# Kernel tuning notes

Measured on AMD Instinct MI355X. Metric: run time of the kernel, lower is better.

Reference implementation:

```python
import jax, jax.numpy as jnp
import numpy as np

EMB_DIM = 1024
NUM_HEAD = 16
HEAD_DIM = EMB_DIM // NUM_HEAD
B, S = 2, 2048


def setup_inputs() -> dict:
    key = jax.random.key(0)
    ks = jax.random.split(key, 10)
    scale = 1.0 / np.sqrt(EMB_DIM)
    x = jax.random.normal(ks[0], (B, S, EMB_DIM), dtype=jnp.float32)
    # causal mask: 1 = keep, 0 = masked out (torch masked_fill(mask == 0, -inf))
    mask = jnp.tril(jnp.ones((S, S), dtype=jnp.int32))[None, None, :, :]
    def lin(kw, kb):
        W = jax.random.uniform(kw, (EMB_DIM, EMB_DIM), jnp.float32, -scale, scale)
        b = jax.random.uniform(kb, (EMB_DIM,), jnp.float32, -scale, scale)
        return W, b
    Wq, bq = lin(ks[1], ks[2])
    Wk, bk = lin(ks[3], ks[4])
    Wv, bv = lin(ks[5], ks[6])
    Wo, bo = lin(ks[7], ks[8])
    return {"x": x, "mask": mask, "Wq": Wq, "bq": bq, "Wk": Wk, "bk": bk,
            "Wv": Wv, "bv": bv, "Wo": Wo, "bo": bo}


def reference(x, mask, Wq, bq, Wk, bk, Wv, bv, Wo, bo):
    Bsz, Sq, _ = x.shape
    # projections; torch Linear: y = x @ W^T + b
    def proj(W, b):
        y = jnp.einsum('bse,fe->bsf', x, W) + b
        return y.reshape(Bsz, Sq, NUM_HEAD, HEAD_DIM).transpose(0, 2, 1, 3)  # [B,H,S,D]
    q = proj(Wq, bq)
    k = proj(Wk, bk)
    v = proj(Wv, bv)
    scaling = jnp.asarray(HEAD_DIM ** 0.5, x.dtype)
    scores = jnp.einsum('bhqd,bhkd->bhqk', q, k) / scaling  # [B,H,S,S]
    scores = jnp.where(mask == 0, -jnp.inf, scores)
    attn = jax.nn.softmax(scores, axis=-1)
    out = jnp.einsum('bhqk,bhkd->bhqd', attn, v)
    out = out.transpose(0, 2, 1, 3).reshape(Bsz, Sq, EMB_DIM)
    return jnp.einsum('bse,fe->bsf', out, Wo) + bo
```

## Files before the change

kernel.cpp:

```cpp
#include <hip/hip_runtime.h>

typedef unsigned short u16;
typedef __attribute__((ext_vector_type(8))) __bf16 bf16x8;
typedef __attribute__((ext_vector_type(8))) short  short8;
typedef __attribute__((ext_vector_type(4))) short  short4v;
typedef __attribute__((ext_vector_type(4))) float  floatx4;
typedef __attribute__((ext_vector_type(4))) int    intx4;
typedef __attribute__((ext_vector_type(2))) int    intx2;

constexpr int Bc = 2, Sc = 2048, Ec = 1024, Hc = 16, Dc = 64;
constexpr int Mc = Bc * Sc;

#define QSCALE  0.18033688011112042f

__device__ __forceinline__ u16 f2b(float f) {
  union { float f; unsigned u; } c; c.f = f;
  unsigned u = c.u;
  return (u16)((u + 0x7fffu + ((u >> 16) & 1u)) >> 16);
}
__device__ __forceinline__ short8 ld8(const u16* p) { return *(const short8*)p; }

__device__ __forceinline__ int cvt_pk(float lo, float hi) {
  int r;
  asm("v_cvt_pk_bf16_f32 %0, %1, %2" : "=v"(r) : "v"(lo), "v"(hi));
  return r;
}

__device__ __forceinline__ floatx4 mfma16(short8 a, short8 b, floatx4 c) {
  return __builtin_amdgcn_mfma_f32_16x16x32_bf16(
      __builtin_bit_cast(bf16x8, a), __builtin_bit_cast(bf16x8, b), c, 0, 0, 0);
}

__device__ __forceinline__ void async16(const u16* g, u16* l) {
  __builtin_amdgcn_global_load_lds(
      (const __attribute__((address_space(1))) void*)g,
      (__attribute__((address_space(3))) void*)l, 16, 0, 0);
}

__global__ __launch_bounds__(256) void cvt_kernel(
    const float* __restrict__ x,  const float* __restrict__ Wq,
    const float* __restrict__ Wk, const float* __restrict__ Wv,
    const float* __restrict__ Wo, u16* __restrict__ dst) {
  const size_t i = ((size_t)blockIdx.x * 256 + threadIdx.x) * 4;
  const int seg = (int)(i >> 20);
  const float* src;
  size_t off;
  if (seg < 4)       { src = x;  off = i; }
  else if (seg == 4) { src = Wq; off = i - ((size_t)4 << 20); }
  else if (seg == 5) { src = Wk; off = i - ((size_t)5 << 20); }
  else if (seg == 6) { src = Wv; off = i - ((size_t)6 << 20); }
  else               { src = Wo; off = i - ((size_t)7 << 20); }
  floatx4 v = *(const floatx4*)(src + off);
  intx2 o;
  o[0] = cvt_pk(v[0], v[1]);
  o[1] = cvt_pk(v[2], v[3]);
  *(intx2*)(dst + i) = o;
}

__device__ __forceinline__ void gemm128d(
    const u16* __restrict__ A, const u16* __restrict__ B, int K,
    int m0, int n0, u16* As, u16* Bs, floatx4 acc[4][4]) {
  const int t = threadIdx.x;
  const int w = t >> 6, lane = t & 63;
  const int wm = w & 1, wn = w >> 1;
  const int quad = lane >> 4, l16 = lane & 15;
  const int r = t >> 2;
  const int c = ((t & 3) ^ ((t >> 3) & 3)) * 8;
  const int rs = (quad ^ ((l16 >> 1) & 3)) * 8;

  const u16* ap0 = A + (size_t)(m0 + r) * K + c;
  const u16* ap1 = A + (size_t)(m0 + 64 + r) * K + c;
  const u16* bp0 = B + (size_t)(n0 + r) * K + c;
  const u16* bp1 = B + (size_t)(n0 + 64 + r) * K + c;
  u16* const al0 = As + w * 512;
  u16* const al1 = As + 2048 + w * 512;
  u16* const bl0 = Bs + w * 512;
  u16* const bl1 = Bs + 2048 + w * 512;

#pragma unroll
  for (int i = 0; i < 4; ++i)
#pragma unroll
    for (int j = 0; j < 4; ++j) acc[i][j] = 0.f;

  async16(ap0, al0);
  async16(ap1, al1);
  async16(bp0, bl0);
  async16(bp1, bl1);

  int cur = 0;
  for (int k0 = 0; k0 < K; k0 += 32) {
    if (k0 + 32 < K) {
      const int nb = cur ^ 1;
      async16(ap0 + k0 + 32, al0 + nb * 4096);
      async16(ap1 + k0 + 32, al1 + nb * 4096);
      async16(bp0 + k0 + 32, bl0 + nb * 4096);
      async16(bp1 + k0 + 32, bl1 + nb * 4096);
      __builtin_amdgcn_sched_barrier(0);
      asm volatile("s_waitcnt vmcnt(4)");
    } else {
      asm volatile("s_waitcnt vmcnt(0)");
    }
    __builtin_amdgcn_s_barrier();
    __builtin_amdgcn_sched_barrier(0);

    short8 af[4], bfr[4];
#pragma unroll
    for (int i = 0; i < 4; ++i)
      af[i]  = *(const short8*)(As + cur * 4096 +
                                (wm * 64 + i * 16 + l16) * 32 + rs);
#pragma unroll
    for (int j = 0; j < 4; ++j)
      bfr[j] = *(const short8*)(Bs + cur * 4096 +
                                (wn * 64 + j * 16 + l16) * 32 + rs);
#pragma unroll
    for (int i = 0; i < 4; ++i)
#pragma unroll
      for (int j = 0; j < 4; ++j)
        acc[i][j] = mfma16(af[i], bfr[j], acc[i][j]);

    __builtin_amdgcn_sched_barrier(0);
    __builtin_amdgcn_s_barrier();
    cur ^= 1;
  }
}

__device__ __forceinline__ void gemm64x128(
    const u16* __restrict__ A, const u16* __restrict__ B, int K,
    int m0, int n0, u16* As, u16* Bs, floatx4 acc[2][4]) {
  const int t = threadIdx.x;
  const int w = t >> 6, lane = t & 63;
  const int wm = w & 1, wn = w >> 1;
  const int quad = lane >> 4, l16 = lane & 15;
  const int r = t >> 2;
  const int c = ((t & 3) ^ ((t >> 3) & 3)) * 8;
  const int rs = (quad ^ ((l16 >> 1) & 3)) * 8;

  const u16* ap  = A + (size_t)(m0 + r) * K + c;
  const u16* bp0 = B + (size_t)(n0 + r) * K + c;
  const u16* bp1 = B + (size_t)(n0 + 64 + r) * K + c;
  u16* const al  = As + w * 512;
  u16* const bl0 = Bs + w * 512;
  u16* const bl1 = Bs + 2048 + w * 512;

#pragma unroll
  for (int i = 0; i < 2; ++i)
#pragma unroll
    for (int j = 0; j < 4; ++j) acc[i][j] = 0.f;

  async16(ap,  al);
  async16(bp0, bl0);
  async16(bp1, bl1);

  int cur = 0;
  for (int k0 = 0; k0 < K; k0 += 32) {
    if (k0 + 32 < K) {
      const int nb = cur ^ 1;
      async16(ap  + k0 + 32, al  + nb * 2048);
      async16(bp0 + k0 + 32, bl0 + nb * 4096);
      async16(bp1 + k0 + 32, bl1 + nb * 4096);
      __builtin_amdgcn_sched_barrier(0);
      asm volatile("s_waitcnt vmcnt(3)");
    } else {
      asm volatile("s_waitcnt vmcnt(0)");
    }
    __builtin_amdgcn_s_barrier();
    __builtin_amdgcn_sched_barrier(0);

    short8 af[2], bfr[4];
#pragma unroll
    for (int i = 0; i < 2; ++i)
      af[i]  = *(const short8*)(As + cur * 2048 +
                                (wm * 32 + i * 16 + l16) * 32 + rs);
#pragma unroll
    for (int j = 0; j < 4; ++j)
      bfr[j] = *(const short8*)(Bs + cur * 4096 +
                                (wn * 64 + j * 16 + l16) * 32 + rs);
#pragma unroll
    for (int i = 0; i < 2; ++i)
#pragma unroll
      for (int j = 0; j < 4; ++j)
        acc[i][j] = mfma16(af[i], bfr[j], acc[i][j]);

    __builtin_amdgcn_sched_barrier(0);
    __builtin_amdgcn_s_barrier();
    cur ^= 1;
  }
}

__global__ __launch_bounds__(256, 4) void qkv_mm(
    const u16* __restrict__ xb, const u16* __restrict__ Wb,
    const float* __restrict__ bq, const float* __restrict__ bk,
    const float* __restrict__ bv,
    u16* __restrict__ Q, u16* __restrict__ K_, u16* __restrict__ Vt) {
  __shared__ __align__(16) u16 As[8192], Bs[8192];
  const int z = blockIdx.z;
  const u16* W = Wb + ((size_t)z << 20);
  const float* bias = (z == 0) ? bq : (z == 1) ? bk : bv;
  const int m0 = blockIdx.y * 128, n0 = blockIdx.x * 128;

  floatx4 acc[4][4];
  gemm128d(xb, W, Ec, m0, n0, As, Bs, acc);

  const int t = threadIdx.x, w = t >> 6, lane = t & 63;
  const int wm = w & 1, wn = w >> 1, quad = lane >> 4, l16 = lane & 15;
#pragma unroll
  for (int i = 0; i < 4; ++i)
#pragma unroll
    for (int j = 0; j < 4; ++j)
#pragma unroll
      for (int rr = 0; rr < 4; ++rr) {
        const int row = m0 + wm * 64 + i * 16 + quad * 4 + rr;
        const int col = n0 + wn * 64 + j * 16 + l16;
        float v = acc[i][j][rr] + bias[col];
        if (z == 0) v *= QSCALE;
        const int bb = row >> 11, s = row & (Sc - 1);
        const int h = col >> 6, d = col & (Dc - 1), bh = bb * Hc + h;
        if (z < 2) ((z == 0) ? Q : K_)[((size_t)bh * Sc + s) * Dc + d] = f2b(v);
        else {
          const int sp = (s & ~31) | ((s & 12) << 1) | ((s & 16) >> 2) | (s & 3);
          Vt[((size_t)bh * Dc + d) * Sc + sp] = f2b(v);
        }
      }
}

__global__ __launch_bounds__(256, 6) void proj_mm(
    const u16* __restrict__ O, const u16* __restrict__ Wob,
    const float* __restrict__ bias, float* __restrict__ out) {
  __shared__ __align__(16) u16 As[4096], Bs[8192];
  const int m0 = blockIdx.y * 64, n0 = blockIdx.x * 128;

  floatx4 acc[2][4];
  gemm64x128(O, Wob, Ec, m0, n0, As, Bs, acc);

  const int t = threadIdx.x, w = t >> 6, lane = t & 63;
  const int wm = w & 1, wn = w >> 1, quad = lane >> 4, l16 = lane & 15;
#pragma unroll
  for (int i = 0; i < 2; ++i)
#pragma unroll
    for (int j = 0; j < 4; ++j)
#pragma unroll
      for (int rr = 0; rr < 4; ++rr) {
        const int row = m0 + wm * 32 + i * 16 + quad * 4 + rr;
        const int col = n0 + wn * 64 + j * 16 + l16;
        out[(size_t)row * Ec + col] = acc[i][j][rr] + bias[col];
      }
}

__global__ __launch_bounds__(512, 4) void attn_kernel(
    const u16* __restrict__ Q, const u16* __restrict__ K,
    const u16* __restrict__ Vt, u16* __restrict__ O) {
  const int id = blockIdx.x;
  int qt, bh;
  if (id < 256) { qt = id & 15;        bh = id >> 4; }
  else          { qt = 15 - (id & 15); bh = 16 + ((id - 256) >> 4); }
  const int q0 = qt * 128;
  const int bb = bh >> 4, h = bh & 15;

  const u16* Qh = Q  + (size_t)bh * Sc * Dc;
  const u16* Kh = K  + (size_t)bh * Sc * Dc;
  const u16* Vh = Vt + (size_t)bh * Dc * Sc;

  const int t = threadIdx.x;
  const int w = t >> 6, lane = t & 63;
  const int quad = lane >> 4, l16 = lane & 15;

  __shared__ __align__(16) u16 Ks[8192];
  __shared__ __align__(16) u16 Vs[8192];

  const int sr = w * 8 + (lane >> 3);
  const int sb = (lane & 7) ^ (lane >> 3);
  const int swz = l16 & 7;

  const u16* qrow_p = Qh + (size_t)(q0 + w * 16 + l16) * Dc;
  const short8 aq0 = ld8(qrow_p + quad * 8);
  const short8 aq1 = ld8(qrow_p + 32 + quad * 8);

  float   lrow = 0.f;
  floatx4 oacc[4];
#pragma unroll
  for (int dt = 0; dt < 4; ++dt) oacc[dt] = 0.f;

  for (int kt = 0; kt <= q0; kt += 128) {
#pragma unroll
    for (int st = 0; st < 2; ++st) {
      async16(Kh + (size_t)(kt + st * 64 + sr) * Dc + sb * 8,
              Ks + st * 4096 + w * 512);
      async16(Vh + (size_t)sr * Sc + kt + st * 64 + sb * 8,
              Vs + st * 4096 + w * 512);
    }
    __syncthreads();

    floatx4 sacc[8];
#pragma unroll
    for (int g = 0; g < 8; ++g) sacc[g] = 0.f;
    __builtin_amdgcn_s_setprio(1);
#pragma unroll
    for (int ks = 0; ks < 2; ++ks) {
      const short8 bq = ks ? aq1 : aq0;
#pragma unroll
      for (int g = 0; g < 8; ++g) {
        const short8 a = *(const short8*)(
            Ks + (g >> 2) * 4096 + ((g & 3) * 16 + l16) * 64 +
            (((ks * 4 + quad) ^ swz) * 8));
        sacc[g] = mfma16(a, bq, sacc[g]);
      }
    }
    __builtin_amdgcn_s_setprio(0);

    const bool diag = (kt == q0);
    const int thr = q0 + w * 16 + l16 - kt - 4 * quad;
#pragma unroll
    for (int g = 0; g < 8; ++g)
#pragma unroll
      for (int r = 0; r < 4; ++r) {
        float pv = exp2f(sacc[g][r]);
        if (diag && (16 * g + r > thr)) pv = 0.f;
        lrow += pv;
        sacc[g][r] = pv;
      }

    short8 pa[4];
#pragma unroll
    for (int c = 0; c < 4; ++c) {
      intx4 wd;
      wd[0] = cvt_pk(sacc[2 * c][0],     sacc[2 * c][1]);
      wd[1] = cvt_pk(sacc[2 * c][2],     sacc[2 * c][3]);
      wd[2] = cvt_pk(sacc[2 * c + 1][0], sacc[2 * c + 1][1]);
      wd[3] = cvt_pk(sacc[2 * c + 1][2], sacc[2 * c + 1][3]);
      pa[c] = __builtin_bit_cast(short8, wd);
    }

    __builtin_amdgcn_s_setprio(1);
#pragma unroll
    for (int c = 0; c < 4; ++c) {
      const int st = c >> 1, kcl = c & 1;
#pragma unroll
      for (int dt = 0; dt < 4; ++dt) {
        const short8 b = *(const short8*)(
            Vs + st * 4096 + (dt * 16 + l16) * 64 +
            (((kcl * 4 + quad) ^ swz) * 8));
        oacc[dt] = mfma16(pa[c], b, oacc[dt]);
      }
    }
    __builtin_amdgcn_s_setprio(0);
    __syncthreads();
  }

  lrow += __shfl_xor(lrow, 16);
  lrow += __shfl_xor(lrow, 32);
  float rs[4];
#pragma unroll
  for (int r = 0; r < 4; ++r)
    rs[r] = 1.f / __shfl(lrow, quad * 4 + r, 16);

#pragma unroll
  for (int dt = 0; dt < 4; ++dt) {
#pragma unroll
    for (int r = 0; r < 4; ++r) {
      const int qrow = q0 + w * 16 + quad * 4 + r;
      O[((size_t)(bb * Sc + qrow)) * Ec + h * Dc + dt * 16 + l16] =
          f2b(oacc[dt][r] * rs[r]);
    }
  }
}

extern "C" void kernel_launch(void* const* d_in, const int* in_sizes, int n_in,
                              void* d_out, int out_size, void* d_ws, size_t ws_size,
                              hipStream_t stream) {
  const float* x  = (const float*)d_in[0];
  const float* Wq = (const float*)d_in[2];
  const float* bq = (const float*)d_in[3];
  const float* Wk = (const float*)d_in[4];
  const float* bk = (const float*)d_in[5];
  const float* Wv = (const float*)d_in[6];
  const float* bv = (const float*)d_in[7];
  const float* Wo = (const float*)d_in[8];
  const float* bo = (const float*)d_in[9];

  const size_t MiE = (size_t)Mc * Ec;
  u16* Q  = (u16*)d_ws;
  u16* K  = Q  + MiE;
  u16* Vt = K  + MiE;
  u16* O  = Vt + MiE;
  u16* xb = O  + MiE;
  u16* Wb = xb + MiE;
  u16* Wob = Wb + ((size_t)3 << 20);

  cvt_kernel<<<8192, 256, 0, stream>>>(x, Wq, Wk, Wv, Wo, xb);
  qkv_mm<<<dim3(Ec / 128, Mc / 128, 3), 256, 0, stream>>>(
      xb, Wb, bq, bk, bv, Q, K, Vt);
  attn_kernel<<<512, 512, 0, stream>>>(Q, K, Vt, O);
  proj_mm<<<dim3(Ec / 128, Mc / 64), 256, 0, stream>>>(O, Wob, bo, (float*)d_out);
}
```

Measured before the change: 203.6 us.

## Double-buffer K/V tiles and give each wave two query row groups

```diff
diff --git a/kernel.cpp b/kernel.cpp
--- a/kernel.cpp
+++ b/kernel.cpp
@@ -246,7 +246,7 @@
       }
 }
 
-__global__ __launch_bounds__(512, 4) void attn_kernel(
+__global__ __launch_bounds__(256, 2) void attn_kernel(
     const u16* __restrict__ Q, const u16* __restrict__ K,
     const u16* __restrict__ Vt, u16* __restrict__ O) {
   const int id = blockIdx.x;
@@ -264,71 +264,101 @@
   const int w = t >> 6, lane = t & 63;
   const int quad = lane >> 4, l16 = lane & 15;
 
-  __shared__ __align__(16) u16 Ks[8192];
-  __shared__ __align__(16) u16 Vs[8192];
+  __shared__ __align__(16) u16 Ks[16384];
+  __shared__ __align__(16) u16 Vs[16384];
 
   const int sr = w * 8 + (lane >> 3);
   const int sb = (lane & 7) ^ (lane >> 3);
   const int swz = l16 & 7;
 
-  const u16* qrow_p = Qh + (size_t)(q0 + w * 16 + l16) * Dc;
-  const short8 aq0 = ld8(qrow_p + quad * 8);
-  const short8 aq1 = ld8(qrow_p + 32 + quad * 8);
-
-  float   lrow = 0.f;
-  floatx4 oacc[4];
-#pragma unroll
-  for (int dt = 0; dt < 4; ++dt) oacc[dt] = 0.f;
-
+  short8 aq[2][2];
+#pragma unroll
+  for (int gq = 0; gq < 2; ++gq) {
+    const u16* qp = Qh + (size_t)(q0 + gq * 64 + w * 16 + l16) * Dc;
+    aq[gq][0] = ld8(qp + quad * 8);
+    aq[gq][1] = ld8(qp + 32 + quad * 8);
+  }
+
+  float   lrow[2] = {0.f, 0.f};
+  floatx4 oacc[2][4];
+#pragma unroll
+  for (int gq = 0; gq < 2; ++gq)
+#pragma unroll
+    for (int dt = 0; dt < 4; ++dt) oacc[gq][dt] = 0.f;
+
+#define ATTN_STAGE(kt_, buf_)                                                  \
+  {                                                                            \
+    _Pragma("unroll")                                                          \
+    for (int st = 0; st < 2; ++st)                                             \
+      _Pragma("unroll")                                                        \
+      for (int it = 0; it < 2; ++it) {                                         \
+        const int r_ = it * 32 + sr;                                           \
+        async16(Kh + (size_t)((kt_) + st * 64 + r_) * Dc + sb * 8,             \
+                Ks + (buf_)*8192 + st * 4096 + it * 2048 + w * 512);           \
+        async16(Vh + (size_t)r_ * Sc + (kt_) + st * 64 + sb * 8,               \
+                Vs + (buf_)*8192 + st * 4096 + it * 2048 + w * 512);           \
+      }                                                                        \
+  }
+
+  ATTN_STAGE(0, 0);
+  int cur = 0;
   for (int kt = 0; kt <= q0; kt += 128) {
-#pragma unroll
-    for (int st = 0; st < 2; ++st) {
-      async16(Kh + (size_t)(kt + st * 64 + sr) * Dc + sb * 8,
-              Ks + st * 4096 + w * 512);
-      async16(Vh + (size_t)sr * Sc + kt + st * 64 + sb * 8,
-              Vs + st * 4096 + w * 512);
-    }
-    __syncthreads();
-
-    floatx4 sacc[8];
-#pragma unroll
-    for (int g = 0; g < 8; ++g) sacc[g] = 0.f;
+    if (kt < q0) {
+      ATTN_STAGE(kt + 128, cur ^ 1);
+      __builtin_amdgcn_sched_barrier(0);
+      asm volatile("s_waitcnt vmcnt(8)");
+    } else {
+      asm volatile("s_waitcnt vmcnt(0)");
+    }
+    __builtin_amdgcn_s_barrier();
+    __builtin_amdgcn_sched_barrier(0);
+
+    floatx4 sacc[2][8];
+#pragma unroll
+    for (int gq = 0; gq < 2; ++gq)
+#pragma unroll
+      for (int g = 0; g < 8; ++g) sacc[gq][g] = 0.f;
     __builtin_amdgcn_s_setprio(1);
 #pragma unroll
     for (int ks = 0; ks < 2; ++ks) {
-      const short8 bq = ks ? aq1 : aq0;
 #pragma unroll
       for (int g = 0; g < 8; ++g) {
         const short8 a = *(const short8*)(
-            Ks + (g >> 2) * 4096 + ((g & 3) * 16 + l16) * 64 +
+            Ks + cur * 8192 + (g >> 2) * 4096 + ((g & 3) * 16 + l16) * 64 +
             (((ks * 4 + quad) ^ swz) * 8));
-        sacc[g] = mfma16(a, bq, sacc[g]);
+        sacc[0][g] = mfma16(a, aq[0][ks], sacc[0][g]);
+        sacc[1][g] = mfma16(a, aq[1][ks], sacc[1][g]);
       }
     }
     __builtin_amdgcn_s_setprio(0);
 
     const bool diag = (kt == q0);
-    const int thr = q0 + w * 16 + l16 - kt - 4 * quad;
-#pragma unroll
-    for (int g = 0; g < 8; ++g)
-#pragma unroll
-      for (int r = 0; r < 4; ++r) {
-        float pv = exp2f(sacc[g][r]);
-        if (diag && (16 * g + r > thr)) pv = 0.f;
-        lrow += pv;
-        sacc[g][r] = pv;
-      }
-
-    short8 pa[4];
-#pragma unroll
-    for (int c = 0; c < 4; ++c) {
-      intx4 wd;
-      wd[0] = cvt_pk(sacc[2 * c][0],     sacc[2 * c][1]);
-      wd[1] = cvt_pk(sacc[2 * c][2],     sacc[2 * c][3]);
-      wd[2] = cvt_pk(sacc[2 * c + 1][0], sacc[2 * c + 1][1]);
-      wd[3] = cvt_pk(sacc[2 * c + 1][2], sacc[2 * c + 1][3]);
-      pa[c] = __builtin_bit_cast(short8, wd);
-    }
+#pragma unroll
+    for (int gq = 0; gq < 2; ++gq) {
+      const int thr = gq * 64 + w * 16 + l16 - 4 * quad;
+#pragma unroll
+      for (int g = 0; g < 8; ++g)
+#pragma unroll
+        for (int r = 0; r < 4; ++r) {
+          float pv = exp2f(sacc[gq][g][r]);
+          if (diag && (16 * g + r > thr)) pv = 0.f;
+          lrow[gq] += pv;
+          sacc[gq][g][r] = pv;
+        }
+    }
+
+    short8 pa[2][4];
+#pragma unroll
+    for (int gq = 0; gq < 2; ++gq)
+#pragma unroll
+      for (int c = 0; c < 4; ++c) {
+        intx4 wd;
+        wd[0] = cvt_pk(sacc[gq][2 * c][0],     sacc[gq][2 * c][1]);
+        wd[1] = cvt_pk(sacc[gq][2 * c][2],     sacc[gq][2 * c][3]);
+        wd[2] = cvt_pk(sacc[gq][2 * c + 1][0], sacc[gq][2 * c + 1][1]);
+        wd[3] = cvt_pk(sacc[gq][2 * c + 1][2], sacc[gq][2 * c + 1][3]);
+        pa[gq][c] = __builtin_bit_cast(short8, wd);
+      }
 
     __builtin_amdgcn_s_setprio(1);
 #pragma unroll
@@ -337,30 +367,35 @@
 #pragma unroll
       for (int dt = 0; dt < 4; ++dt) {
         const short8 b = *(const short8*)(
-            Vs + st * 4096 + (dt * 16 + l16) * 64 +
+            Vs + cur * 8192 + st * 4096 + (dt * 16 + l16) * 64 +
             (((kcl * 4 + quad) ^ swz) * 8));
-        oacc[dt] = mfma16(pa[c], b, oacc[dt]);
+        oacc[0][dt] = mfma16(pa[0][c], b, oacc[0][dt]);
+        oacc[1][dt] = mfma16(pa[1][c], b, oacc[1][dt]);
       }
     }
     __builtin_amdgcn_s_setprio(0);
-    __syncthreads();
-  }
-
-  lrow += __shfl_xor(lrow, 16);
-  lrow += __shfl_xor(lrow, 32);
-  float rs[4];
-#pragma unroll
-  for (int r = 0; r < 4; ++r)
-    rs[r] = 1.f / __shfl(lrow, quad * 4 + r, 16);
-
-#pragma unroll
-  for (int dt = 0; dt < 4; ++dt) {
-#pragma unroll
-    for (int r = 0; r < 4; ++r) {
-      const int qrow = q0 + w * 16 + quad * 4 + r;
-      O[((size_t)(bb * Sc + qrow)) * Ec + h * Dc + dt * 16 + l16] =
-          f2b(oacc[dt][r] * rs[r]);
-    }
+
+    __builtin_amdgcn_sched_barrier(0);
+    __builtin_amdgcn_s_barrier();
+    cur ^= 1;
+  }
+
+#pragma unroll
+  for (int gq = 0; gq < 2; ++gq) {
+    lrow[gq] += __shfl_xor(lrow[gq], 16);
+    lrow[gq] += __shfl_xor(lrow[gq], 32);
+    float rs[4];
+#pragma unroll
+    for (int r = 0; r < 4; ++r)
+      rs[r] = 1.f / __shfl(lrow[gq], quad * 4 + r, 16);
+#pragma unroll
+    for (int dt = 0; dt < 4; ++dt)
+#pragma unroll
+      for (int r = 0; r < 4; ++r) {
+        const int qrow = q0 + gq * 64 + w * 16 + quad * 4 + r;
+        O[((size_t)(bb * Sc + qrow)) * Ec + h * Dc + dt * 16 + l16] =
+            f2b(oacc[gq][dt][r] * rs[r]);
+      }
   }
 }
 
@@ -389,6 +424,6 @@
   cvt_kernel<<<8192, 256, 0, stream>>>(x, Wq, Wk, Wv, Wo, xb);
   qkv_mm<<<dim3(Ec / 128, Mc / 128, 3), 256, 0, stream>>>(
       xb, Wb, bq, bk, bv, Q, K, Vt);
-  attn_kernel<<<512, 512, 0, stream>>>(Q, K, Vt, O);
+  attn_kernel<<<512, 256, 0, stream>>>(Q, K, Vt, O);
   proj_mm<<<dim3(Ec / 128, Mc / 64), 256, 0, stream>>>(O, Wob, bo, (float*)d_out);
 }
```

Result: no change. 205.1 us (+0.7%).
